# Optimization experiments

Hardware: AMD Instinct MI355X
Metric: run time of the kernel (lower is better)

Reference implementation:

```python
import jax, jax.numpy as jnp
import numpy as np

VOCAB = 32000
HIDDEN = 1024
BATCH = 32
SEQ = 128


def setup_inputs() -> dict:
    key = jax.random.key(0)
    ks = jax.random.split(key, 8)
    p = lambda k, shape: (jax.random.normal(k, shape, dtype=jnp.float32) * 0.01)
    return {
        "x": jax.random.randint(ks[0], (BATCH, SEQ), 0, VOCAB, dtype=jnp.int64),
        "state": jnp.zeros((BATCH, HIDDEN), dtype=jnp.float32),
        "W_xr": p(ks[1], (VOCAB, HIDDEN)),
        "W_hr": p(ks[2], (HIDDEN, HIDDEN)),
        "b_r": jnp.zeros((HIDDEN,), dtype=jnp.float32),
        "W_xz": p(ks[3], (VOCAB, HIDDEN)),
        "W_hz": p(ks[4], (HIDDEN, HIDDEN)),
        "b_z": jnp.zeros((HIDDEN,), dtype=jnp.float32),
        "W_xh": p(ks[5], (VOCAB, HIDDEN)),
        "W_hh": p(ks[6], (HIDDEN, HIDDEN)),
        "b_h": jnp.zeros((HIDDEN,), dtype=jnp.float32),
        "W_ho": p(ks[7], (HIDDEN, VOCAB)),
        "b_o": jnp.zeros((VOCAB,), dtype=jnp.float32),
    }


def reference(x, state, W_xr, W_hr, b_r, W_xz, W_hz, b_z, W_xh, W_hh, b_h, W_ho, b_o):
    # x: (B, T) int tokens -> transpose to (T, B) like torch `x.T`.
    # one_hot(tok) @ W_x* is mathematically an embedding row gather: W_x*[tok].
    tokens = x.T  # (T, B)

    def step(h, tok):
        xr = W_xr[tok]  # (B, H)
        xz = W_xz[tok]
        xh = W_xh[tok]
        r = jax.nn.sigmoid(xr + h @ W_hr + b_r)
        z = jax.nn.sigmoid(xz + h @ W_hz + b_z)
        cand = jnp.tanh(xh + (r * h) @ W_hh + b_h)
        h_new = z * h + (1.0 - z) * cand
        out = h_new @ W_ho + b_o  # (B, V)
        return h_new, out

    final_state, outs = jax.lax.scan(step, state, tokens)  # outs: (T, B, V)
    # torch.cat(outputs, dim=0) concatenates per-step (B, V) blocks -> (T*B, V)
    return outs.reshape(-1, outs.shape[-1]), final_state
```

## Files before the change

kernel.cpp:

```cpp
#include <hip/hip_runtime.h>
#include <hip/hip_bf16.h>
#include <cstdint>
#include <cstddef>

#define VOCAB 32000
#define HIDDEN 1024
#define BATCH 32
#define SEQ 128

typedef __attribute__((ext_vector_type(8))) short short8v;
typedef __attribute__((ext_vector_type(4))) float float4v;
typedef __attribute__((ext_vector_type(2))) unsigned int uint2v;

__device__ __forceinline__ unsigned short f2bf(float f) {
    unsigned int x = __float_as_uint(f);
    unsigned int r = x + 0x7fffu + ((x >> 16) & 1u);
    return (unsigned short)(r >> 16);
}

__global__ __launch_bounds__(256) void k_transpose_bf(const float* __restrict__ in,
                                                      unsigned short* __restrict__ out,
                                                      int cols, int rows) {
    __shared__ float tile[64][65];
    const int jb = blockIdx.x;
    const int kb = blockIdx.y;
    const int t  = threadIdx.x;
    const int c  = t & 63;
    const int r0 = (t >> 6) * 16;
#pragma unroll
    for (int i = 0; i < 16; i++) {
        int r = r0 + i;
        tile[r][c] = in[(size_t)(kb * 64 + r) * cols + jb * 64 + c];
    }
    __syncthreads();
#pragma unroll
    for (int i = 0; i < 16; i++) {
        int r = r0 + i;
        out[(size_t)(jb * 64 + r) * rows + kb * 64 + c] = f2bf(tile[c][r]);
    }
}

__global__ __launch_bounds__(256) void k_init_hbf(const float* __restrict__ state,
                                                  unsigned short* __restrict__ hinit) {
    int i = blockIdx.x * 256 + threadIdx.x;
    if (i < BATCH * HIDDEN) hinit[i] = f2bf(state[i]);
}


#define WAIT_VM0 asm volatile("s_waitcnt vmcnt(0)" ::: "memory")
#define LGKM0    asm volatile("s_waitcnt lgkmcnt(0)" ::: "memory")

#define ST8_WT(P, V) \
    asm volatile("global_store_dwordx2 %0, %1, off sc0 sc1" ::"v"(P), "v"(V) : "memory")

__device__ __forceinline__ void row_poll(const unsigned int* row, unsigned int tag) {
    const unsigned int* p = row + (threadIdx.x & 63);
    int guard = 0;
    while (true) {
        unsigned int v = __hip_atomic_load(p, __ATOMIC_RELAXED, __HIP_MEMORY_SCOPE_AGENT);
        if (__all((int)(v >= tag))) break;
        if (++guard > 8192) break;
        __builtin_amdgcn_s_sleep(1);
    }
}

__global__ __launch_bounds__(64, 1) void k_rnn(const int* __restrict__ x,
                                               const float* __restrict__ state,
                                               const unsigned short* __restrict__ wrt,
                                               const unsigned short* __restrict__ wzt,
                                               const unsigned short* __restrict__ wht,
                                               const float* __restrict__ W_xr, const float* __restrict__ b_r,
                                               const float* __restrict__ W_xz, const float* __restrict__ b_z,
                                               const float* __restrict__ W_xh, const float* __restrict__ b_h,
                                               const unsigned short* __restrict__ hinit,
                                               unsigned short* __restrict__ hall,
                                               unsigned short* __restrict__ rhall,
                                               float* __restrict__ hstate_out,
                                               unsigned int* __restrict__ mbox) {
    const int bid = blockIdx.x;
    const int g   = bid >> 6;
    const int jsl = bid & 63;
    const int j0  = jsl * 16;
    const int b0  = g * 16;
    const int l   = threadIdx.x;
    const int llo = l & 15;
    const int lhi = l >> 4;
    const int jg  = j0 + llo;

    unsigned int* gm           = mbox + g * 64 * 64;
    const unsigned int* myrow  = gm + jsl * 64;
    unsigned int* pushtgt      = gm + l * 64 + jsl;

    __shared__ short8v wlds[3][32][64];
    __shared__ int xs[16 * SEQ];
    __shared__ unsigned short pack[16 * 16];

#pragma unroll
    for (int i = 0; i < 32; i++) {
        const size_t off = (size_t)jg * HIDDEN + i * 32 + lhi * 8;
        wlds[0][i][l] = *(const short8v*)&wrt[off];
        wlds[1][i][l] = *(const short8v*)&wzt[off];
        wlds[2][i][l] = *(const short8v*)&wht[off];
    }
    for (int i = l; i < 16 * SEQ; i += 64)
        xs[i] = x[(size_t)(b0 + (i >> 7)) * SEQ + (i & 127)];

    const float brv = b_r[jg], bzv = b_z[jg], bhv = b_h[jg];
    float4v hO;
#pragma unroll
    for (int q = 0; q < 4; q++) hO[q] = state[(b0 + 4 * lhi + q) * HIDDEN + jg];
    LGKM0;

    for (int t = 0; t < SEQ; t++) {
        const unsigned short* hprev =
            t ? (hall + (size_t)(t - 1) * BATCH * HIDDEN) : hinit;
        unsigned short* rhp = rhall + (size_t)t * BATCH * HIDDEN;
        unsigned short* hp  = hall + (size_t)t * BATCH * HIDDEN;

        int tok[4];
#pragma unroll
        for (int q = 0; q < 4; q++) tok[q] = xs[(4 * lhi + q) * SEQ + t];
        float xr[4], xz[4], xh[4];
#pragma unroll
        for (int q = 0; q < 4; q++) {
            xr[q] = W_xr[(size_t)tok[q] * HIDDEN + jg];
            xz[q] = W_xz[(size_t)tok[q] * HIDDEN + jg];
            xh[q] = W_xh[(size_t)tok[q] * HIDDEN + jg];
        }

        if (t) row_poll(myrow, 2u * (unsigned)t);

        short8v af[32];
#pragma unroll
        for (int i = 0; i < 32; i++)
            af[i] = *(const short8v*)&hprev[(b0 + llo) * HIDDEN + i * 32 + lhi * 8];

        float4v aR0 = {0.f, 0.f, 0.f, 0.f}, aR1 = {0.f, 0.f, 0.f, 0.f};
        float4v aZ0 = {0.f, 0.f, 0.f, 0.f}, aZ1 = {0.f, 0.f, 0.f, 0.f};
#pragma unroll
        for (int i = 0; i < 32; i += 2) {
            aR0 = __builtin_amdgcn_mfma_f32_16x16x32_bf16(af[i],     wlds[0][i][l],     aR0, 0, 0, 0);
            aZ0 = __builtin_amdgcn_mfma_f32_16x16x32_bf16(af[i],     wlds[1][i][l],     aZ0, 0, 0, 0);
            aR1 = __builtin_amdgcn_mfma_f32_16x16x32_bf16(af[i + 1], wlds[0][i + 1][l], aR1, 0, 0, 0);
            aZ1 = __builtin_amdgcn_mfma_f32_16x16x32_bf16(af[i + 1], wlds[1][i + 1][l], aZ1, 0, 0, 0);
        }

        float4v zv;
#pragma unroll
        for (int q = 0; q < 4; q++) {
            float sr = aR0[q] + aR1[q] + xr[q] + brv;
            float sz = aZ0[q] + aZ1[q] + xz[q] + bzv;
            float rv = 1.f / (1.f + __expf(-sr));
            zv[q]    = 1.f / (1.f + __expf(-sz));
            pack[(4 * lhi + q) * 16 + llo] = f2bf(rv * hO[q]);
        }
        LGKM0;
        __builtin_amdgcn_wave_barrier();
        {
            uint2v v = *(const uint2v*)&pack[(l >> 2) * 16 + (l & 3) * 4];
            ST8_WT(&rhp[(b0 + (l >> 2)) * HIDDEN + j0 + (l & 3) * 4], v);
            WAIT_VM0;
            __hip_atomic_store(pushtgt, 2u * (unsigned)t + 1u, __ATOMIC_RELAXED,
                               __HIP_MEMORY_SCOPE_AGENT);
        }

        row_poll(myrow, 2u * (unsigned)t + 1u);

        short8v ar[32];
#pragma unroll
        for (int i = 0; i < 32; i++)
            ar[i] = *(const short8v*)&rhp[(b0 + llo) * HIDDEN + i * 32 + lhi * 8];

        float4v aC0 = {0.f, 0.f, 0.f, 0.f}, aC1 = {0.f, 0.f, 0.f, 0.f};
#pragma unroll
        for (int i = 0; i < 32; i += 2) {
            aC0 = __builtin_amdgcn_mfma_f32_16x16x32_bf16(ar[i],     wlds[2][i][l],     aC0, 0, 0, 0);
            aC1 = __builtin_amdgcn_mfma_f32_16x16x32_bf16(ar[i + 1], wlds[2][i + 1][l], aC1, 0, 0, 0);
        }
#pragma unroll
        for (int q = 0; q < 4; q++) {
            float a = aC0[q] + aC1[q] + xh[q] + bhv;
            a = fminf(15.f, fmaxf(-15.f, a));
            float e2   = __expf(2.f * a);
            float cand = (e2 - 1.f) / (e2 + 1.f);
            float hn   = zv[q] * hO[q] + (1.f - zv[q]) * cand;
            hO[q]      = hn;
            pack[(4 * lhi + q) * 16 + llo] = f2bf(hn);
        }
        LGKM0;
        __builtin_amdgcn_wave_barrier();
        {
            uint2v v = *(const uint2v*)&pack[(l >> 2) * 16 + (l & 3) * 4];
            ST8_WT(&hp[(b0 + (l >> 2)) * HIDDEN + j0 + (l & 3) * 4], v);
            WAIT_VM0;
            __hip_atomic_store(pushtgt, 2u * (unsigned)t + 2u, __ATOMIC_RELAXED,
                               __HIP_MEMORY_SCOPE_AGENT);
        }
    }

#pragma unroll
    for (int q = 0; q < 4; q++)
        hstate_out[(b0 + 4 * lhi + q) * HIDDEN + jg] = hO[q];
}

#define BM 128
#define BN 128
#define BK 64

__device__ __forceinline__ void gload_lds16(const void* g, void* l) {
    __builtin_amdgcn_global_load_lds((const __attribute__((address_space(1))) void*)g,
                                     (__attribute__((address_space(3))) void*)l, 16, 0, 0);
}

__global__ __launch_bounds__(256, 2) void k_gemm(const unsigned short* __restrict__ A,
                                                 const unsigned short* __restrict__ B,
                                                 const float* __restrict__ bo,
                                                 float* __restrict__ out) {
    __shared__ unsigned short As[BM * BK];
    __shared__ unsigned short Bs[BN * BK];
    const int wg   = blockIdx.y * 250 + blockIdx.x;
    const int swz  = (wg & 7) * 1000 + (wg >> 3);
    const int nb   = swz % 250;
    const int mb   = swz / 250;
    const int tid  = threadIdx.x;
    const int lane = tid & 63;
    const int w    = tid >> 6;
    const int wm   = w >> 1, wn = w & 1;
    const int row0 = mb * BM, col0 = nb * BN;

    float4v acc[4][4];
#pragma unroll
    for (int i = 0; i < 4; i++)
#pragma unroll
        for (int j = 0; j < 4; j++) acc[i][j] = float4v{0.f, 0.f, 0.f, 0.f};

    for (int kt = 0; kt < HIDDEN / BK; kt++) {
#pragma unroll
        for (int i = 0; i < 4; i++) {
            int s   = i * 256 + tid;
            int row = s >> 3;
            int off = (s & 7) * 8;
            gload_lds16(A + (size_t)(row0 + row) * HIDDEN + kt * BK + off, &As[s * 8]);
            gload_lds16(B + (size_t)(col0 + row) * HIDDEN + kt * BK + off, &Bs[s * 8]);
        }
        __syncthreads();
#pragma unroll
        for (int kk = 0; kk < 2; kk++) {
            short8v af[4], bf[4];
#pragma unroll
            for (int i = 0; i < 4; i++) {
                int ar = wm * 64 + i * 16 + (lane & 15);
                af[i] = *(short8v*)&As[ar * BK + kk * 32 + (lane >> 4) * 8];
                int br = wn * 64 + i * 16 + (lane & 15);
                bf[i] = *(short8v*)&Bs[br * BK + kk * 32 + (lane >> 4) * 8];
            }
#pragma unroll
            for (int i = 0; i < 4; i++)
#pragma unroll
                for (int j = 0; j < 4; j++)
                    acc[i][j] = __builtin_amdgcn_mfma_f32_16x16x32_bf16(af[i], bf[j], acc[i][j], 0, 0, 0);
        }
        __syncthreads();
    }
#pragma unroll
    for (int i = 0; i < 4; i++) {
        int grow = row0 + wm * 64 + i * 16 + (lane >> 4) * 4;
#pragma unroll
        for (int j = 0; j < 4; j++) {
            int gcol   = col0 + wn * 64 + j * 16 + (lane & 15);
            float bias = bo[gcol];
#pragma unroll
            for (int r = 0; r < 4; r++) {
                __builtin_nontemporal_store(acc[i][j][r] + bias,
                                            &out[(size_t)(grow + r) * VOCAB + gcol]);
            }
        }
    }
}


extern "C" void kernel_launch(void* const* d_in, const int* in_sizes, int n_in,
                              void* d_out, int out_size, void* d_ws, size_t ws_size,
                              hipStream_t stream) {
    const int*   x     = (const int*)d_in[0];
    const float* state = (const float*)d_in[1];
    const float* W_xr  = (const float*)d_in[2];
    const float* W_hr  = (const float*)d_in[3];
    const float* b_r   = (const float*)d_in[4];
    const float* W_xz  = (const float*)d_in[5];
    const float* W_hz  = (const float*)d_in[6];
    const float* b_z   = (const float*)d_in[7];
    const float* W_xh  = (const float*)d_in[8];
    const float* W_hh  = (const float*)d_in[9];
    const float* b_h   = (const float*)d_in[10];
    const float* W_ho  = (const float*)d_in[11];
    const float* b_o   = (const float*)d_in[12];

    float* out    = (float*)d_out;
    float* hstate = out + (size_t)SEQ * BATCH * VOCAB;

    char* ws = (char*)d_ws;
    unsigned short* hall  = (unsigned short*)ws;
    unsigned short* rhall = (unsigned short*)(ws + 8388608);
    unsigned short* bt    = (unsigned short*)(ws + 16777216);
    unsigned short* wrt   = (unsigned short*)(ws + 82313216);
    unsigned short* wzt   = (unsigned short*)(ws + 84410368);
    unsigned short* wht   = (unsigned short*)(ws + 86507520);
    unsigned short* hinit = (unsigned short*)(ws + 88604672);
    unsigned int*   mbox  = (unsigned int*)(ws + 88670208);

    hipMemsetAsync(mbox, 0, 32768, stream);
    k_transpose_bf<<<dim3(16, 16), 256, 0, stream>>>(W_hr, wrt, HIDDEN, HIDDEN);
    k_transpose_bf<<<dim3(16, 16), 256, 0, stream>>>(W_hz, wzt, HIDDEN, HIDDEN);
    k_transpose_bf<<<dim3(16, 16), 256, 0, stream>>>(W_hh, wht, HIDDEN, HIDDEN);
    k_transpose_bf<<<dim3(500, 16), 256, 0, stream>>>(W_ho, bt, VOCAB, HIDDEN);
    k_init_hbf<<<128, 256, 0, stream>>>(state, hinit);

    k_rnn<<<128, 64, 0, stream>>>(x, state, wrt, wzt, wht, W_xr, b_r, W_xz, b_z, W_xh, b_h,
                                  hinit, hall, rhall, hstate, mbox);

    k_gemm<<<dim3(250, 32), 256, 0, stream>>>(hall, bt, b_o, out);
}
```

Baseline: 1.288 ms.

## Rewrite output GEMM as 256x256 double-buffered 8-wave kernel with swizzled LDS

Replaces the 128x128 single-buffer output GEMM with a 256x256-tile, 512-thread kernel. It double-buffers K tiles in LDS, staging half-tiles between MFMA phases with barriers and priority hints, and XOR-swizzles the LDS layout to avoid bank conflicts. The aim is to overlap global loads with MFMA work, cut the number of synchronisation stalls, and raise operand reuse per block. The large LDS footprint limits occupancy, and the extra barriers add sync cost.

```diff
diff --git a/kernel.cpp b/kernel.cpp
--- a/kernel.cpp
+++ b/kernel.cpp
@@ -203,77 +203,181 @@
         hstate_out[(b0 + 4 * lhi + q) * HIDDEN + jg] = hO[q];
 }
 
-#define BM 128
-#define BN 128
-#define BK 64
+#define GTM 16
+#define GTN 125
 
 __device__ __forceinline__ void gload_lds16(const void* g, void* l) {
     __builtin_amdgcn_global_load_lds((const __attribute__((address_space(1))) void*)g,
                                      (__attribute__((address_space(3))) void*)l, 16, 0, 0);
 }
 
-__global__ __launch_bounds__(256, 2) void k_gemm(const unsigned short* __restrict__ A,
-                                                 const unsigned short* __restrict__ B,
-                                                 const float* __restrict__ bo,
-                                                 float* __restrict__ out) {
-    __shared__ unsigned short As[BM * BK];
-    __shared__ unsigned short Bs[BN * BK];
-    const int wg   = blockIdx.y * 250 + blockIdx.x;
-    const int swz  = (wg & 7) * 1000 + (wg >> 3);
-    const int nb   = swz % 250;
-    const int mb   = swz / 250;
-    const int tid  = threadIdx.x;
-    const int lane = tid & 63;
-    const int w    = tid >> 6;
-    const int wm   = w >> 1, wn = w & 1;
-    const int row0 = mb * BM, col0 = nb * BN;
-
-    float4v acc[4][4];
-#pragma unroll
-    for (int i = 0; i < 4; i++)
+__device__ __forceinline__ void stage_half(const unsigned short* __restrict__ mbase,
+                                           unsigned short* ldsm, int half, int isB,
+                                           int kt, int tid) {
+#pragma unroll
+    for (int i = 0; i < 2; i++) {
+        int s  = i * 512 + tid;
+        int ri = s >> 3;
+        int cb = (s & 7) * 16;
+        int rt = isB ? ((ri >> 5) * 64 + half * 32 + (ri & 31))
+                     : ((ri >> 6) * 128 + half * 64 + (ri & 63));
+        int cbs = cb ^ ((rt & 7) << 4);
+        gload_lds16(mbase + (size_t)rt * HIDDEN + kt * 64 + (cbs >> 1),
+                    ldsm + rt * 64 + (cb >> 1));
+    }
+}
+
+__global__ __launch_bounds__(512, 2) void k_gemm8(const unsigned short* __restrict__ A,
+                                                  const unsigned short* __restrict__ B,
+                                                  const float* __restrict__ bo,
+                                                  float* __restrict__ out) {
+    __shared__ unsigned short lds[2][2][256 * 64];
+
+    const int wg   = blockIdx.x;
+    const int swz  = (wg & 7) * 250 + (wg >> 3);
+    const int mb   = swz / GTN;
+    const int nb   = swz % GTN;
+    const int row0 = mb * 256, col0 = nb * 256;
+
+    const int tid = threadIdx.x;
+    const int w   = tid >> 6;
+    const int wm  = w >> 2;
+    const int wn  = w & 3;
+    const int l   = tid & 63;
+    const int llo = l & 15;
+    const int lhi = l >> 4;
+
+    const unsigned short* Ab = A + (size_t)row0 * HIDDEN;
+    const unsigned short* Bb = B + (size_t)col0 * HIDDEN;
+
+    float4v acc[8][4];
+#pragma unroll
+    for (int i = 0; i < 8; i++)
 #pragma unroll
         for (int j = 0; j < 4; j++) acc[i][j] = float4v{0.f, 0.f, 0.f, 0.f};
 
-    for (int kt = 0; kt < HIDDEN / BK; kt++) {
-#pragma unroll
-        for (int i = 0; i < 4; i++) {
-            int s   = i * 256 + tid;
-            int row = s >> 3;
-            int off = (s & 7) * 8;
-            gload_lds16(A + (size_t)(row0 + row) * HIDDEN + kt * BK + off, &As[s * 8]);
-            gload_lds16(B + (size_t)(col0 + row) * HIDDEN + kt * BK + off, &Bs[s * 8]);
-        }
-        __syncthreads();
-#pragma unroll
-        for (int kk = 0; kk < 2; kk++) {
-            short8v af[4], bf[4];
-#pragma unroll
-            for (int i = 0; i < 4; i++) {
-                int ar = wm * 64 + i * 16 + (lane & 15);
-                af[i] = *(short8v*)&As[ar * BK + kk * 32 + (lane >> 4) * 8];
-                int br = wn * 64 + i * 16 + (lane & 15);
-                bf[i] = *(short8v*)&Bs[br * BK + kk * 32 + (lane >> 4) * 8];
+    stage_half(Ab, &lds[0][0][0], 0, 0, 0, tid);
+    stage_half(Bb, &lds[0][1][0], 0, 1, 0, tid);
+    stage_half(Ab, &lds[0][0][0], 1, 0, 0, tid);
+    stage_half(Bb, &lds[0][1][0], 1, 1, 0, tid);
+    stage_half(Ab, &lds[1][0][0], 0, 0, 1, tid);
+    stage_half(Bb, &lds[1][1][0], 0, 1, 1, tid);
+    asm volatile("s_waitcnt vmcnt(4)" ::: "memory");
+    __builtin_amdgcn_s_barrier();
+
+    for (int kt = 0; kt < 16; kt++) {
+        unsigned short* lA = &lds[kt & 1][0][0];
+        unsigned short* lB = &lds[kt & 1][1][0];
+        unsigned short* nA = &lds[(kt & 1) ^ 1][0][0];
+        unsigned short* nB = &lds[(kt & 1) ^ 1][1][0];
+        short8v afr[4][2];
+        short8v bfr[2][2][2];
+
+#pragma unroll
+        for (int mfq = 0; mfq < 4; mfq++)
+#pragma unroll
+            for (int ks = 0; ks < 2; ks++) {
+                int rt = wm * 128 + mfq * 16 + llo;
+                int cb = ks * 64 + lhi * 16;
+                afr[mfq][ks] = *(const short8v*)&lA[rt * 64 + ((cb ^ ((rt & 7) << 4)) >> 1)];
             }
 #pragma unroll
-            for (int i = 0; i < 4; i++)
-#pragma unroll
-                for (int j = 0; j < 4; j++)
-                    acc[i][j] = __builtin_amdgcn_mfma_f32_16x16x32_bf16(af[i], bf[j], acc[i][j], 0, 0, 0);
-        }
-        __syncthreads();
-    }
-#pragma unroll
-    for (int i = 0; i < 4; i++) {
-        int grow = row0 + wm * 64 + i * 16 + (lane >> 4) * 4;
-#pragma unroll
-        for (int j = 0; j < 4; j++) {
-            int gcol   = col0 + wn * 64 + j * 16 + (lane & 15);
+        for (int nfq = 0; nfq < 2; nfq++)
+#pragma unroll
+            for (int ks = 0; ks < 2; ks++) {
+                int rt = wn * 64 + nfq * 16 + llo;
+                int cb = ks * 64 + lhi * 16;
+                bfr[0][nfq][ks] = *(const short8v*)&lB[rt * 64 + ((cb ^ ((rt & 7) << 4)) >> 1)];
+            }
+        if (kt + 1 < 16) stage_half(Ab, nA, 1, 0, kt + 1, tid);
+        __builtin_amdgcn_s_barrier();
+        __builtin_amdgcn_s_setprio(1);
+#pragma unroll
+        for (int mfq = 0; mfq < 4; mfq++)
+#pragma unroll
+            for (int nfq = 0; nfq < 2; nfq++)
+#pragma unroll
+                for (int ks = 0; ks < 2; ks++)
+                    acc[mfq][nfq] = __builtin_amdgcn_mfma_f32_16x16x32_bf16(
+                        afr[mfq][ks], bfr[0][nfq][ks], acc[mfq][nfq], 0, 0, 0);
+        __builtin_amdgcn_s_setprio(0);
+        __builtin_amdgcn_s_barrier();
+
+#pragma unroll
+        for (int nfq = 0; nfq < 2; nfq++)
+#pragma unroll
+            for (int ks = 0; ks < 2; ks++) {
+                int rt = wn * 64 + 32 + nfq * 16 + llo;
+                int cb = ks * 64 + lhi * 16;
+                bfr[1][nfq][ks] = *(const short8v*)&lB[rt * 64 + ((cb ^ ((rt & 7) << 4)) >> 1)];
+            }
+        if (kt + 1 < 16) stage_half(Bb, nB, 1, 1, kt + 1, tid);
+        __builtin_amdgcn_s_barrier();
+        __builtin_amdgcn_s_setprio(1);
+#pragma unroll
+        for (int mfq = 0; mfq < 4; mfq++)
+#pragma unroll
+            for (int nfq = 0; nfq < 2; nfq++)
+#pragma unroll
+                for (int ks = 0; ks < 2; ks++)
+                    acc[mfq][2 + nfq] = __builtin_amdgcn_mfma_f32_16x16x32_bf16(
+                        afr[mfq][ks], bfr[1][nfq][ks], acc[mfq][2 + nfq], 0, 0, 0);
+        __builtin_amdgcn_s_setprio(0);
+        __builtin_amdgcn_s_barrier();
+
+#pragma unroll
+        for (int mfq = 0; mfq < 4; mfq++)
+#pragma unroll
+            for (int ks = 0; ks < 2; ks++) {
+                int rt = wm * 128 + 64 + mfq * 16 + llo;
+                int cb = ks * 64 + lhi * 16;
+                afr[mfq][ks] = *(const short8v*)&lA[rt * 64 + ((cb ^ ((rt & 7) << 4)) >> 1)];
+            }
+        if (kt + 2 < 16) stage_half(Ab, lA, 0, 0, kt + 2, tid);
+        __builtin_amdgcn_s_barrier();
+        __builtin_amdgcn_s_setprio(1);
+#pragma unroll
+        for (int mfq = 0; mfq < 4; mfq++)
+#pragma unroll
+            for (int nfq = 0; nfq < 2; nfq++)
+#pragma unroll
+                for (int ks = 0; ks < 2; ks++)
+                    acc[4 + mfq][nfq] = __builtin_amdgcn_mfma_f32_16x16x32_bf16(
+                        afr[mfq][ks], bfr[0][nfq][ks], acc[4 + mfq][nfq], 0, 0, 0);
+        __builtin_amdgcn_s_setprio(0);
+        __builtin_amdgcn_s_barrier();
+
+        if (kt + 2 < 16) stage_half(Bb, lB, 0, 1, kt + 2, tid);
+        __builtin_amdgcn_s_barrier();
+        __builtin_amdgcn_s_setprio(1);
+#pragma unroll
+        for (int mfq = 0; mfq < 4; mfq++)
+#pragma unroll
+            for (int nfq = 0; nfq < 2; nfq++)
+#pragma unroll
+                for (int ks = 0; ks < 2; ks++)
+                    acc[4 + mfq][2 + nfq] = __builtin_amdgcn_mfma_f32_16x16x32_bf16(
+                        afr[mfq][ks], bfr[1][nfq][ks], acc[4 + mfq][2 + nfq], 0, 0, 0);
+        __builtin_amdgcn_s_setprio(0);
+        if (kt + 2 < 16) {
+            asm volatile("s_waitcnt vmcnt(4)" ::: "memory");
+        } else if (kt + 1 < 16) {
+            asm volatile("s_waitcnt vmcnt(0)" ::: "memory");
+        }
+        __builtin_amdgcn_s_barrier();
+    }
+
+#pragma unroll
+    for (int mf = 0; mf < 8; mf++) {
+        int grow = row0 + wm * 128 + mf * 16 + lhi * 4;
+#pragma unroll
+        for (int nf = 0; nf < 4; nf++) {
+            int gcol   = col0 + wn * 64 + nf * 16 + llo;
             float bias = bo[gcol];
 #pragma unroll
-            for (int r = 0; r < 4; r++) {
-                __builtin_nontemporal_store(acc[i][j][r] + bias,
+            for (int r = 0; r < 4; r++)
+                __builtin_nontemporal_store(acc[mf][nf][r] + bias,
                                             &out[(size_t)(grow + r) * VOCAB + gcol]);
-            }
         }
     }
 }
@@ -319,5 +423,5 @@
     k_rnn<<<128, 64, 0, stream>>>(x, state, wrt, wzt, wht, W_xr, b_r, W_xz, b_z, W_xh, b_h,
                                   hinit, hall, rhall, hstate, mbox);
 
-    k_gemm<<<dim3(250, 32), 256, 0, stream>>>(hall, bt, b_o, out);
-}
+    k_gemm8<<<dim3(2000), 512, 0, stream>>>(hall, bt, b_o, out);
+}
```

Result: faster. 1.204 ms (-6.5%).
